# Performance work log

Hardware: AMD Instinct MI355X
Metric: run time of the kernel (lower is better)

## Reference

```python
import jax, jax.numpy as jnp
import numpy as np

N, E, IN_DIM, HID, HEADS, OUT_DIM, T = 50000, 200000, 32, 64, 4, 32, 3
NEG_SLOPE = 0.2  # PyG GATv2Conv default


def setup_inputs() -> dict:
    key = jax.random.key(0)
    ks = jax.random.split(key, 16)
    s = 0.1
    return {
        "feat": jax.random.normal(ks[0], (N, IN_DIM), jnp.float32),
        "W_in": jax.random.normal(ks[1], (IN_DIM, HID), jnp.float32) * s,
        "b_in": jnp.zeros((HID,), jnp.float32),
        "Wl": jax.random.normal(ks[2], (2 * HID, HEADS * HID), jnp.float32) * s,
        "bl": jnp.zeros((HEADS * HID,), jnp.float32),
        "Wr": jax.random.normal(ks[3], (2 * HID, HEADS * HID), jnp.float32) * s,
        "br": jnp.zeros((HEADS * HID,), jnp.float32),
        "att": jax.random.normal(ks[4], (HEADS, HID), jnp.float32) * s,
        "b_conv": jnp.zeros((HEADS * HID,), jnp.float32),
        "Wg": jax.random.normal(ks[5], (HID, OUT_DIM), jnp.float32) * s,
        "bg": jnp.zeros((OUT_DIM,), jnp.float32),
        "edge_index": jax.random.randint(ks[6], (2, E), 0, N, jnp.int32),
        "node_mask": jax.random.randint(ks[7], (N,), 0, T + 1, jnp.int32),
        "current_state": jax.random.randint(ks[8], (N,), 0, 2, jnp.int32),
    }


def reference(feat, W_in, b_in, Wl, bl, Wr, br, att, b_conv, Wg, bg,
              edge_index, node_mask, current_state):
    # add self loops (GATv2Conv add_self_loops=True)
    loops = jnp.arange(N, dtype=edge_index.dtype)
    src = jnp.concatenate([edge_index[0], loops])  # [E+N]
    dst = jnp.concatenate([edge_index[1], loops])

    h0 = feat @ W_in + b_in  # [N, HID]
    bias_sum = b_conv.reshape(HEADS, HID).sum(0)  # heads are summed after bias add

    def step(h, i):
        active = node_mask > i  # [N] bool: nodes updated at this step
        x = jnp.concatenate([h, h0], axis=-1)  # [N, 2*HID]
        xl = (x @ Wl + bl).reshape(N, HEADS, HID)  # source transform
        xr = (x @ Wr + br).reshape(N, HEADS, HID)  # target transform
        e_act = active[src] & active[dst]  # edge alive iff both endpoints active
        s = jax.nn.leaky_relu(xl[src] + xr[dst], NEG_SLOPE)  # [E+N, H, C]
        score = jnp.einsum('ehc,hc->eh', s, att)  # [E+N, H]
        score = jnp.where(e_act[:, None], score, -1e30)
        smax = jax.lax.stop_gradient(
            jax.ops.segment_max(score, dst, num_segments=N))  # [N, H]
        ex = jnp.exp(score - smax[dst]) * e_act[:, None].astype(score.dtype)
        denom = jax.ops.segment_sum(ex, dst, num_segments=N)  # [N, H]
        alpha = ex / jnp.maximum(denom[dst], 1e-16)  # segment softmax per dst
        msg = alpha[:, :, None] * xl[src]  # [E+N, H, C]
        agg = jax.ops.segment_sum(msg, dst, num_segments=N)  # [N, H, C]
        out = jnp.tanh(agg.sum(1) + bias_sum)  # sum over heads, then Tanh
        return jnp.where(active[:, None], out, h), None

    h, _ = jax.lax.scan(step, h0, jnp.arange(T))
    # original returns g_embed(h[current_state]); fixed-shape variant: mask rows
    out = (h @ Wg + bg) * (current_state[:, None] > 0).astype(h.dtype)
    return out
```

## Files before the change

### kernel.cpp

```cpp
#include <hip/hip_runtime.h>
#include <hip/hip_bf16.h>

#define NN      50000
#define EE      200000
#define IN_DIM  32
#define HID     64
#define HEADS   4
#define OUTD    32
#define TSTEPS  3

typedef unsigned short bf16_t;
typedef __attribute__((ext_vector_type(8))) short  short8;
typedef __attribute__((ext_vector_type(4))) float  floatx4;

__device__ __forceinline__ float b2f(bf16_t u) {
    union { unsigned int i; float f; } v; v.i = ((unsigned int)u) << 16; return v.f;
}
__device__ __forceinline__ bf16_t f2b(float f) {
    union { float f; unsigned int i; } v; v.f = f;
    unsigned int r = v.i + 0x7FFF + ((v.i >> 16) & 1);
    return (bf16_t)(r >> 16);
}

__global__ __launch_bounds__(256) void k_setup(
        const void* W_in, const void* b_in, const void* att, const void* bconv,
        const void* Wg, const void* bg,
        const void* Wl_raw, const void* Wr_raw, const void* bl_raw, const void* br_raw,
        float* Winf, float* binf, float* attf, float* bcf, float* Wgf, float* bgf,
        bf16_t* __restrict__ Wt, float* __restrict__ bb,
        int* __restrict__ deg, int* __restrict__ flag, int* __restrict__ mbuf) {
    __shared__ int bad;
    int t = threadIdx.x, bid = blockIdx.x;
    if (t == 0) bad = 0;
    __syncthreads();
    {
        const bf16_t* p = (const bf16_t*)W_in;
        int mybad = 0;
        for (int i = t; i < IN_DIM * HID; i += 256) {
            float v = b2f(p[i]);
            if (v != v || fabsf(v) > 100.f) mybad = 1;
        }
        if (mybad) atomicOr(&bad, 1);
    }
    __syncthreads();
    int f = bad ? 0 : 1;
    if (bid == 0 && t == 0) *flag = f;

    if (bid < 256) {
        int i = bid * 256 + t;
        int n = i >> 7, k = i & 127;
        const void* W = (n < 256) ? Wl_raw : Wr_raw;
        int nn = (n < 256) ? n : n - 256;
        float v = f ? b2f(((const bf16_t*)W)[k * 256 + nn])
                    : ((const float*)W)[k * 256 + nn];
        Wt[i] = f2b(v);
        if (k == 0) {
            const void* b = (n < 256) ? bl_raw : br_raw;
            bb[n] = f ? b2f(((const bf16_t*)b)[nn]) : ((const float*)b)[nn];
        }
    } else if (bid < 275) {
        int i = (bid - 256) * 256 + t;
        const void* src; float* dst; int off;
        if      (i < 2048) { src = W_in;  dst = Winf; off = i; }
        else if (i < 2112) { src = b_in;  dst = binf; off = i - 2048; }
        else if (i < 2368) { src = att;   dst = attf; off = i - 2112; }
        else if (i < 2624) { src = bconv; dst = bcf;  off = i - 2368; }
        else if (i < 4672) { src = Wg;    dst = Wgf;  off = i - 2624; }
        else if (i < 4704) { src = bg;    dst = bgf;  off = i - 4672; }
        else return;
        dst[off] = f ? b2f(((const bf16_t*)src)[off]) : ((const float*)src)[off];
    } else {
        int i = (bid - 275) * 256 + t;
        if (i < NN) deg[i] = 0;
        if (bid == 275 && t < 16) mbuf[t] = 0;
    }
}

__global__ __launch_bounds__(256) void k_hist_all(const int* __restrict__ dst,
                                                  const int* __restrict__ mask,
                                                  int* __restrict__ deg,
                                                  int* __restrict__ mbuf) {
    int t = threadIdx.x, bid = blockIdx.x;
    int i = bid * 256 + t;
    if (i < EE) atomicAdd(&deg[dst[i]], 1);
    if (bid < (NN + 255) / 256) {
        __shared__ int wcnt[4][4];
        int wid = t >> 6, lane = t & 63;
        int ni = bid * 256 + t;
        bool valid = ni < NN;
        int v = 0;
        if (valid) { int m = mask[ni]; v = m < 0 ? 0 : (m > 3 ? 3 : m); }
#pragma unroll
        for (int b = 0; b < 4; b++) {
            unsigned long long mm = __ballot(valid && v == b);
            if (lane == 0) wcnt[wid][b] = __popcll(mm);
        }
        __syncthreads();
        if (t < 4) {
            int s = wcnt[0][t] + wcnt[1][t] + wcnt[2][t] + wcnt[3][t];
            if (s) atomicAdd(&mbuf[t], s);
        }
    }
}

__global__ __launch_bounds__(256) void k_scan_partial(const int* __restrict__ deg,
                                                      int* __restrict__ part, int n) {
    __shared__ int sd[256];
    int t = threadIdx.x;
    int base = blockIdx.x * 1024;
    int s = 0;
#pragma unroll
    for (int j = 0; j < 4; j++) {
        int i = base + t * 4 + j;
        if (i < n) s += deg[i];
    }
    sd[t] = s; __syncthreads();
    for (int off = 128; off > 0; off >>= 1) {
        if (t < off) sd[t] += sd[t + off];
        __syncthreads();
    }
    if (t == 0) part[blockIdx.x] = sd[0];
}

__global__ void k_scan_mid(int* part, int nch, int* mbuf) {
    if (threadIdx.x == 0 && blockIdx.x == 0) {
        int acc = 0;
        for (int i = 0; i < nch; i++) { int v = part[i]; part[i] = acc; acc += v; }
        part[nch] = acc;
        int c1 = mbuf[1], c2 = mbuf[2], c3 = mbuf[3];
        mbuf[7] = 0;
        mbuf[6] = c3;
        mbuf[5] = c3 + c2;
        mbuf[4] = c3 + c2 + c1;
        mbuf[8] = c3 + c2 + c1;
        mbuf[9] = c3 + c2;
        mbuf[10] = c3;
    }
}

__global__ __launch_bounds__(256) void k_scan_final(const int* __restrict__ deg,
                                                    const int* __restrict__ part,
                                                    int* __restrict__ row_ptr,
                                                    int* __restrict__ cursor,
                                                    int n, int nch) {
    __shared__ int sc[256];
    int t = threadIdx.x;
    int base = blockIdx.x * 1024;
    int v[4]; int s = 0;
#pragma unroll
    for (int j = 0; j < 4; j++) {
        int i = base + t * 4 + j;
        v[j] = (i < n) ? deg[i] : 0;
        s += v[j];
    }
    sc[t] = s; __syncthreads();
    for (int off = 1; off < 256; off <<= 1) {
        int add = (t >= off) ? sc[t - off] : 0;
        __syncthreads();
        sc[t] += add;
        __syncthreads();
    }
    int run = sc[t] - s + part[blockIdx.x];
#pragma unroll
    for (int j = 0; j < 4; j++) {
        int i = base + t * 4 + j;
        if (i < n) { row_ptr[i] = run; cursor[i] = run; run += v[j]; }
    }
    if (blockIdx.x == 0 && t == 0) row_ptr[n] = part[nch];
}

__global__ __launch_bounds__(256) void k_scatter_all(const int* __restrict__ src,
                                                     const int* __restrict__ dst,
                                                     int* __restrict__ cursor,
                                                     int* __restrict__ col,
                                                     const int* __restrict__ mask,
                                                     int* __restrict__ mbuf,
                                                     int* __restrict__ order) {
    int t = threadIdx.x, bid = blockIdx.x;
    int i = bid * 256 + t;
    if (i < EE) {
        int d = dst[i];
        int pos = atomicAdd(&cursor[d], 1);
        col[pos] = src[i];
    }
    if (bid < (NN + 255) / 256) {
        __shared__ int wcnt[4][4];
        __shared__ int bbase[4];
        int wid = t >> 6, lane = t & 63;
        int ni = bid * 256 + t;
        bool valid = ni < NN;
        int v = 0;
        if (valid) { int m = mask[ni]; v = m < 0 ? 0 : (m > 3 ? 3 : m); }
        int rank = 0;
#pragma unroll
        for (int b = 0; b < 4; b++) {
            unsigned long long mm = __ballot(valid && v == b);
            if (valid && v == b)
                rank = __popcll(mm & ((lane == 0) ? 0ull : (~0ull >> (64 - lane))));
            if (lane == 0) wcnt[wid][b] = __popcll(mm);
        }
        __syncthreads();
        if (t < 4) {
            int tot = wcnt[0][t] + wcnt[1][t] + wcnt[2][t] + wcnt[3][t];
            bbase[t] = atomicAdd(&mbuf[4 + t], tot);
        }
        __syncthreads();
        if (valid) {
            int wpre = 0;
            for (int ww = 0; ww < wid; ww++) wpre += wcnt[ww][v];
            order[bbase[v] + wpre + rank] = ni;
        }
    }
}

__global__ __launch_bounds__(256) void k_h0(const void* __restrict__ feat_raw,
                                            const float* __restrict__ W_in,
                                            const float* __restrict__ b_in,
                                            bf16_t* __restrict__ h0,
                                            bf16_t* __restrict__ h,
                                            const int* __restrict__ flag) {
    __shared__ float Ws[IN_DIM * HID];
    __shared__ float bs[HID];
    int t = threadIdx.x;
    for (int i = t; i < IN_DIM * HID; i += 256) Ws[i] = W_in[i];
    if (t < HID) bs[t] = b_in[t];
    __syncthreads();
    int node = blockIdx.x * 4 + (t >> 6);
    int c = t & 63;
    if (node >= NN) return;
    int f = *flag;
    float acc = bs[c];
    if (f) {
        const bf16_t* fr = (const bf16_t*)feat_raw + (size_t)node * IN_DIM;
#pragma unroll
        for (int k = 0; k < IN_DIM; k++) acc += b2f(fr[k]) * Ws[k * HID + c];
    } else {
        const float* fr = (const float*)feat_raw + (size_t)node * IN_DIM;
#pragma unroll
        for (int k = 0; k < IN_DIM; k++) acc += fr[k] * Ws[k * HID + c];
    }
    bf16_t o = f2b(acc);
    h0[(size_t)node * HID + c] = o;
    h [(size_t)node * HID + c] = o;
}

__global__ __launch_bounds__(256) void k_gemm_mfma(const bf16_t* __restrict__ h,
                                                   const bf16_t* __restrict__ h0,
                                                   const bf16_t* __restrict__ Wt,
                                                   const float* __restrict__ bb,
                                                   bf16_t* __restrict__ xl,
                                                   bf16_t* __restrict__ xr,
                                                   const int* __restrict__ order,
                                                   const int* __restrict__ mbuf,
                                                   int step) {
    int count = mbuf[8 + step];
    int mbase = blockIdx.x * 64;
    if (mbase >= count) return;

    __shared__ bf16_t smem[64 * 136 + 128 * 136];
    bf16_t* As = smem;
    bf16_t* Bs = smem + 64 * 136;
    bf16_t* Cs = smem;

    int t = threadIdx.x;
    int nbase = blockIdx.y * 128;

    {
        int ln = t >> 2, lq = t & 3;
        int idx = mbase + ln;
        int node = (idx < count) ? order[idx] : -1;
        ulonglong2 z; z.x = 0; z.y = 0;
#pragma unroll
        for (int j = 0; j < 2; j++) {
            int chunk = lq + j * 4;
            ulonglong2 vh = z, vh0 = z;
            if (node >= 0) {
                vh  = *(const ulonglong2*)(h  + (size_t)node * HID + chunk * 8);
                vh0 = *(const ulonglong2*)(h0 + (size_t)node * HID + chunk * 8);
            }
            *(ulonglong2*)(&As[ln * 136 + chunk * 8]) = vh;
            *(ulonglong2*)(&As[ln * 136 + 64 + chunk * 8]) = vh0;
        }
    }
#pragma unroll
    for (int i = 0; i < 8; i++) {
        int c = t + i * 256;
        int n = c >> 4, kc = (c & 15) * 8;
        *(ulonglong2*)(&Bs[n * 136 + kc]) =
            *(const ulonglong2*)(Wt + (size_t)(nbase + n) * 128 + kc);
    }
    __syncthreads();

    int wv = t >> 6;
    int lane = t & 63;
    int mrow = lane & 15;
    int quad = lane >> 4;

    floatx4 acc[8];
#pragma unroll
    for (int nf = 0; nf < 8; nf++) acc[nf] = (floatx4){0.f, 0.f, 0.f, 0.f};

#pragma unroll
    for (int kq = 0; kq < 4; kq++) {
        short8 a = *(const short8*)(&As[(wv * 16 + mrow) * 136 + kq * 32 + quad * 8]);
#pragma unroll
        for (int nf = 0; nf < 8; nf++) {
            short8 b = *(const short8*)(&Bs[(nf * 16 + mrow) * 136 + kq * 32 + quad * 8]);
            acc[nf] = __builtin_amdgcn_mfma_f32_16x16x32_bf16(a, b, acc[nf], 0, 0, 0);
        }
    }
    __syncthreads();

#pragma unroll
    for (int nf = 0; nf < 8; nf++) {
        float bv = bb[nbase + nf * 16 + mrow];
#pragma unroll
        for (int r = 0; r < 4; r++) {
            int m = wv * 16 + quad * 4 + r;
            Cs[m * 136 + nf * 16 + mrow] = f2b(acc[nf][r] + bv);
        }
    }
    __syncthreads();

    bf16_t* outp = (blockIdx.y < 2) ? xl : xr;
    int cc = (blockIdx.y & 1) * 128;
#pragma unroll
    for (int i = 0; i < 4; i++) {
        int c = t + i * 256;
        int m = c >> 4, kc = (c & 15) * 8;
        int idx = mbase + m;
        if (idx < count) {
            int node = order[idx];
            *(ulonglong2*)(outp + (size_t)node * 256 + cc + kc) =
                *(const ulonglong2*)(&Cs[m * 136 + kc]);
        }
    }
}

__global__ __launch_bounds__(256) void k_agg(bf16_t* __restrict__ h,
                                             const bf16_t* __restrict__ xl,
                                             const bf16_t* __restrict__ xr,
                                             const float* __restrict__ att,
                                             const float* __restrict__ b_conv,
                                             const int* __restrict__ row_ptr,
                                             const int* __restrict__ col,
                                             const int* __restrict__ node_mask,
                                             const int* __restrict__ order,
                                             const int* __restrict__ mbuf,
                                             int step) {
    int wid = threadIdx.x >> 6;
    int lane = threadIdx.x & 63;
    int idx = blockIdx.x * 4 + wid;
    if (idx >= mbuf[8 + step]) return;
    int node = order[idx];

    float4 attv = *(const float4*)(att + lane * 4);
    ushort4 xru = *(const ushort4*)(xr + (size_t)node * 256 + lane * 4);
    float xr0 = b2f(xru.x), xr1 = b2f(xru.y), xr2 = b2f(xru.z), xr3 = b2f(xru.w);

    float a0 = 0.f, a1 = 0.f, a2 = 0.f, a3 = 0.f, l = 0.f;

    auto edge_body = [&](int s, bool act) {
        if (!act) return;
        ushort4 xu = *(const ushort4*)(xl + (size_t)s * 256 + lane * 4);
        float x0 = b2f(xu.x), x1 = b2f(xu.y), x2 = b2f(xu.z), x3 = b2f(xu.w);
        float v0 = x0 + xr0; v0 = v0 > 0.f ? v0 : 0.2f * v0;
        float v1 = x1 + xr1; v1 = v1 > 0.f ? v1 : 0.2f * v1;
        float v2 = x2 + xr2; v2 = v2 > 0.f ? v2 : 0.2f * v2;
        float v3 = x3 + xr3; v3 = v3 > 0.f ? v3 : 0.2f * v3;
        float part = attv.x * v0 + attv.y * v1 + attv.z * v2 + attv.w * v3;
        part += __shfl_xor(part, 1, 64);
        part += __shfl_xor(part, 2, 64);
        part += __shfl_xor(part, 4, 64);
        part += __shfl_xor(part, 8, 64);
        float p = __expf(part);
        l += p;
        a0 += p * x0; a1 += p * x1; a2 += p * x2; a3 += p * x3;
    };

    edge_body(node, true);
    int e0 = row_ptr[node], e1 = row_ptr[node + 1];
    int e = e0;
    for (; e + 1 < e1; e += 2) {
        int s0 = col[e], s1 = col[e + 1];
        int m0 = node_mask[s0], m1 = node_mask[s1];
        edge_body(s0, m0 > step);
        edge_body(s1, m1 > step);
    }
    if (e < e1) {
        int s0 = col[e];
        edge_body(s0, node_mask[s0] > step);
    }

    float inv = 1.f / l;
    float4 bcv = *(const float4*)(b_conv + lane * 4);
    float t0 = a0 * inv + bcv.x;
    float t1 = a1 * inv + bcv.y;
    float t2 = a2 * inv + bcv.z;
    float t3 = a3 * inv + bcv.w;
    t0 += __shfl_xor(t0, 16, 64); t0 += __shfl_xor(t0, 32, 64);
    t1 += __shfl_xor(t1, 16, 64); t1 += __shfl_xor(t1, 32, 64);
    t2 += __shfl_xor(t2, 16, 64); t2 += __shfl_xor(t2, 32, 64);
    t3 += __shfl_xor(t3, 16, 64); t3 += __shfl_xor(t3, 32, 64);
    if (lane < 16) {
        ushort4 o;
        o.x = f2b(tanhf(t0)); o.y = f2b(tanhf(t1));
        o.z = f2b(tanhf(t2)); o.w = f2b(tanhf(t3));
        *(ushort4*)(h + (size_t)node * HID + lane * 4) = o;
    }
}

__global__ __launch_bounds__(256) void k_out(const bf16_t* __restrict__ h,
                                             const float* __restrict__ Wg,
                                             const float* __restrict__ bg,
                                             const int* __restrict__ cs,
                                             void* __restrict__ out,
                                             const int* __restrict__ flag) {
    __shared__ float Ws[HID * OUTD];
    __shared__ float bs[OUTD];
    int t = threadIdx.x;
    for (int i = t; i < HID * OUTD; i += 256) Ws[i] = Wg[i];
    if (t < OUTD) bs[t] = bg[t];
    __syncthreads();
    int node = blockIdx.x * 8 + (t >> 5);
    int c = t & 31;
    if (node >= NN) return;
    float res = 0.f;
    if (cs[node] > 0) {
        const bf16_t* hr = h + (size_t)node * HID;
        float acc = bs[c];
#pragma unroll
        for (int k = 0; k < HID; k++) acc += b2f(hr[k]) * Ws[k * OUTD + c];
        res = acc;
    }
    size_t idx = (size_t)node * OUTD + c;
    if (*flag) ((bf16_t*)out)[idx] = f2b(res);
    else       ((float*)out)[idx]  = res;
}

static inline size_t alignup(size_t x) { return (x + 255) & ~(size_t)255; }

extern "C" void kernel_launch(void* const* d_in, const int* in_sizes, int n_in,
                              void* d_out, int out_size, void* d_ws, size_t ws_size,
                              hipStream_t stream) {
    const void* feat_raw  = d_in[0];
    const void* W_in_raw  = d_in[1];
    const void* b_in_raw  = d_in[2];
    const void* Wl_raw    = d_in[3];
    const void* bl_raw    = d_in[4];
    const void* Wr_raw    = d_in[5];
    const void* br_raw    = d_in[6];
    const void* att_raw   = d_in[7];
    const void* bconv_raw = d_in[8];
    const void* Wg_raw    = d_in[9];
    const void* bg_raw    = d_in[10];
    const int* edge       = (const int*)d_in[11];
    const int* nmask      = (const int*)d_in[12];
    const int* cstate     = (const int*)d_in[13];

    const int* e_src = edge;
    const int* e_dst = edge + EE;

    const size_t SZ_HB   = alignup((size_t)NN * HID * sizeof(bf16_t));
    const size_t SZ_X    = alignup((size_t)NN * 256 * sizeof(bf16_t));
    const size_t SZ_I    = alignup((size_t)NN * sizeof(int));
    const size_t SZ_RP   = alignup((size_t)(NN + 1) * sizeof(int));
    const size_t SZ_COL  = alignup((size_t)EE * sizeof(int));
    const int nch = (NN + 1023) / 1024;
    const size_t SZ_PART = alignup((size_t)(nch + 1) * sizeof(int));
    const size_t SZ_WIN  = alignup((size_t)IN_DIM * HID * sizeof(float));
    const size_t SZ_WT   = alignup((size_t)512 * 128 * sizeof(bf16_t));
    const size_t SZ_B    = alignup(512 * sizeof(float));
    const size_t SZ_WG   = alignup((size_t)HID * OUTD * sizeof(float));

    char* w = (char*)d_ws;
    bf16_t* h0   = (bf16_t*)w; w += SZ_HB;
    bf16_t* h    = (bf16_t*)w; w += SZ_HB;
    bf16_t* xl   = (bf16_t*)w; w += SZ_X;
    bf16_t* xr   = (bf16_t*)w; w += SZ_X;
    int* deg     = (int*)w;    w += SZ_I;
    int* row_ptr = (int*)w;    w += SZ_RP;
    int* cursor  = (int*)w;    w += SZ_I;
    int* colA    = (int*)w;    w += SZ_COL;
    int* order   = (int*)w;    w += SZ_I;
    int* part    = (int*)w;    w += SZ_PART;
    float* Winf  = (float*)w;  w += SZ_WIN;
    bf16_t* Wt   = (bf16_t*)w; w += SZ_WT;
    float* bb    = (float*)w;  w += SZ_B;
    float* attf  = (float*)w;  w += SZ_B;
    float* bcf   = (float*)w;  w += SZ_B;
    float* Wgf   = (float*)w;  w += SZ_WG;
    float* binf  = (float*)w;  w += SZ_B;
    float* bgf   = (float*)w;  w += SZ_B;
    int* flag    = (int*)w;    w += 256;
    int* mbuf    = (int*)w;    w += 256;
    if ((size_t)(w - (char*)d_ws) > ws_size) return;

    k_setup<<<275 + (NN + 255) / 256, 256, 0, stream>>>(
        W_in_raw, b_in_raw, att_raw, bconv_raw, Wg_raw, bg_raw,
        Wl_raw, Wr_raw, bl_raw, br_raw,
        Winf, binf, attf, bcf, Wgf, bgf, Wt, bb, deg, flag, mbuf);

    k_hist_all<<<(EE + 255) / 256, 256, 0, stream>>>(e_dst, nmask, deg, mbuf);
    k_scan_partial<<<nch, 256, 0, stream>>>(deg, part, NN);
    k_scan_mid<<<1, 64, 0, stream>>>(part, nch, mbuf);
    k_scan_final<<<nch, 256, 0, stream>>>(deg, part, row_ptr, cursor, NN, nch);
    k_scatter_all<<<(EE + 255) / 256, 256, 0, stream>>>(e_src, e_dst, cursor, colA,
                                                        nmask, mbuf, order);

    k_h0<<<(NN + 3) / 4, 256, 0, stream>>>(feat_raw, Winf, binf, h0, h, flag);

    for (int s = 0; s < TSTEPS; s++) {
        k_gemm_mfma<<<dim3((NN + 63) / 64, 4), 256, 0, stream>>>(h, h0, Wt, bb, xl, xr,
                                                                 order, mbuf, s);
        k_agg<<<(NN + 3) / 4, 256, 0, stream>>>(h, xl, xr, attf, bcf,
                                                row_ptr, colA, nmask, order, mbuf, s);
    }

    k_out<<<(NN + 7) / 8, 256, 0, stream>>>(h, Wgf, bgf, cstate, d_out, flag);
}
```

Baseline: 277.8 us.

## Pack source activity level into CSR column bits and grid-stride aggregation

The scatter stage now stores each edge's clamped source node_mask in the top bits of the CSR column entry, so the aggregation kernel no longer does a dependent gather of node_mask per edge. The aggregation kernel becomes a persistent grid-stride loop over 2048 blocks, hoisting the att and bias loads, and unrolls the edge loop by four. This removes one indirect load per edge and the launch cost of blocks that would exit immediately. The packing assumes node ids fit in 28 bits and mask values are clamped to 0..3; with a fixed grid, per-wave load balance depends on how nodes are striped.

```diff
diff --git a/kernel.cpp b/kernel.cpp
--- a/kernel.cpp
+++ b/kernel.cpp
@@ -179,9 +179,11 @@
     int t = threadIdx.x, bid = blockIdx.x;
     int i = bid * 256 + t;
     if (i < EE) {
+        int sv = src[i];
+        int m = mask[sv]; m = m < 0 ? 0 : (m > 3 ? 3 : m);
         int d = dst[i];
         int pos = atomicAdd(&cursor[d], 1);
-        col[pos] = src[i];
+        col[pos] = sv | (m << 28);
     }
     if (bid < (NN + 255) / 256) {
         __shared__ int wcnt[4][4];
@@ -344,69 +346,70 @@
                                              const float* __restrict__ b_conv,
                                              const int* __restrict__ row_ptr,
                                              const int* __restrict__ col,
-                                             const int* __restrict__ node_mask,
                                              const int* __restrict__ order,
                                              const int* __restrict__ mbuf,
                                              int step) {
+    int count = mbuf[8 + step];
     int wid = threadIdx.x >> 6;
     int lane = threadIdx.x & 63;
-    int idx = blockIdx.x * 4 + wid;
-    if (idx >= mbuf[8 + step]) return;
-    int node = order[idx];
-
     float4 attv = *(const float4*)(att + lane * 4);
-    ushort4 xru = *(const ushort4*)(xr + (size_t)node * 256 + lane * 4);
-    float xr0 = b2f(xru.x), xr1 = b2f(xru.y), xr2 = b2f(xru.z), xr3 = b2f(xru.w);
-
-    float a0 = 0.f, a1 = 0.f, a2 = 0.f, a3 = 0.f, l = 0.f;
-
-    auto edge_body = [&](int s, bool act) {
-        if (!act) return;
-        ushort4 xu = *(const ushort4*)(xl + (size_t)s * 256 + lane * 4);
-        float x0 = b2f(xu.x), x1 = b2f(xu.y), x2 = b2f(xu.z), x3 = b2f(xu.w);
-        float v0 = x0 + xr0; v0 = v0 > 0.f ? v0 : 0.2f * v0;
-        float v1 = x1 + xr1; v1 = v1 > 0.f ? v1 : 0.2f * v1;
-        float v2 = x2 + xr2; v2 = v2 > 0.f ? v2 : 0.2f * v2;
-        float v3 = x3 + xr3; v3 = v3 > 0.f ? v3 : 0.2f * v3;
-        float part = attv.x * v0 + attv.y * v1 + attv.z * v2 + attv.w * v3;
-        part += __shfl_xor(part, 1, 64);
-        part += __shfl_xor(part, 2, 64);
-        part += __shfl_xor(part, 4, 64);
-        part += __shfl_xor(part, 8, 64);
-        float p = __expf(part);
-        l += p;
-        a0 += p * x0; a1 += p * x1; a2 += p * x2; a3 += p * x3;
-    };
-
-    edge_body(node, true);
-    int e0 = row_ptr[node], e1 = row_ptr[node + 1];
-    int e = e0;
-    for (; e + 1 < e1; e += 2) {
-        int s0 = col[e], s1 = col[e + 1];
-        int m0 = node_mask[s0], m1 = node_mask[s1];
-        edge_body(s0, m0 > step);
-        edge_body(s1, m1 > step);
-    }
-    if (e < e1) {
-        int s0 = col[e];
-        edge_body(s0, node_mask[s0] > step);
-    }
-
-    float inv = 1.f / l;
-    float4 bcv = *(const float4*)(b_conv + lane * 4);
-    float t0 = a0 * inv + bcv.x;
-    float t1 = a1 * inv + bcv.y;
-    float t2 = a2 * inv + bcv.z;
-    float t3 = a3 * inv + bcv.w;
-    t0 += __shfl_xor(t0, 16, 64); t0 += __shfl_xor(t0, 32, 64);
-    t1 += __shfl_xor(t1, 16, 64); t1 += __shfl_xor(t1, 32, 64);
-    t2 += __shfl_xor(t2, 16, 64); t2 += __shfl_xor(t2, 32, 64);
-    t3 += __shfl_xor(t3, 16, 64); t3 += __shfl_xor(t3, 32, 64);
-    if (lane < 16) {
-        ushort4 o;
-        o.x = f2b(tanhf(t0)); o.y = f2b(tanhf(t1));
-        o.z = f2b(tanhf(t2)); o.w = f2b(tanhf(t3));
-        *(ushort4*)(h + (size_t)node * HID + lane * 4) = o;
+    float4 bcv  = *(const float4*)(b_conv + lane * 4);
+
+    for (int idx = blockIdx.x * 4 + wid; idx < count; idx += gridDim.x * 4) {
+        int node = order[idx];
+
+        ushort4 xru = *(const ushort4*)(xr + (size_t)node * 256 + lane * 4);
+        float xr0 = b2f(xru.x), xr1 = b2f(xru.y), xr2 = b2f(xru.z), xr3 = b2f(xru.w);
+
+        float a0 = 0.f, a1 = 0.f, a2 = 0.f, a3 = 0.f, l = 0.f;
+
+        auto do_edge = [&](int s) {
+            ushort4 xu = *(const ushort4*)(xl + (size_t)s * 256 + lane * 4);
+            float x0 = b2f(xu.x), x1 = b2f(xu.y), x2 = b2f(xu.z), x3 = b2f(xu.w);
+            float v0 = x0 + xr0; v0 = v0 > 0.f ? v0 : 0.2f * v0;
+            float v1 = x1 + xr1; v1 = v1 > 0.f ? v1 : 0.2f * v1;
+            float v2 = x2 + xr2; v2 = v2 > 0.f ? v2 : 0.2f * v2;
+            float v3 = x3 + xr3; v3 = v3 > 0.f ? v3 : 0.2f * v3;
+            float part = attv.x * v0 + attv.y * v1 + attv.z * v2 + attv.w * v3;
+            part += __shfl_xor(part, 1, 64);
+            part += __shfl_xor(part, 2, 64);
+            part += __shfl_xor(part, 4, 64);
+            part += __shfl_xor(part, 8, 64);
+            float p = __expf(part);
+            l += p;
+            a0 += p * x0; a1 += p * x1; a2 += p * x2; a3 += p * x3;
+        };
+
+        do_edge(node);
+        int e0 = row_ptr[node], e1 = row_ptr[node + 1];
+        int e = e0;
+        for (; e + 3 < e1; e += 4) {
+            int c0 = col[e], c1 = col[e + 1], c2 = col[e + 2], c3 = col[e + 3];
+            if (((unsigned)c0 >> 28) > (unsigned)step) do_edge(c0 & 0x0FFFFFFF);
+            if (((unsigned)c1 >> 28) > (unsigned)step) do_edge(c1 & 0x0FFFFFFF);
+            if (((unsigned)c2 >> 28) > (unsigned)step) do_edge(c2 & 0x0FFFFFFF);
+            if (((unsigned)c3 >> 28) > (unsigned)step) do_edge(c3 & 0x0FFFFFFF);
+        }
+        for (; e < e1; e++) {
+            int c = col[e];
+            if (((unsigned)c >> 28) > (unsigned)step) do_edge(c & 0x0FFFFFFF);
+        }
+
+        float inv = 1.f / l;
+        float t0 = a0 * inv + bcv.x;
+        float t1 = a1 * inv + bcv.y;
+        float t2 = a2 * inv + bcv.z;
+        float t3 = a3 * inv + bcv.w;
+        t0 += __shfl_xor(t0, 16, 64); t0 += __shfl_xor(t0, 32, 64);
+        t1 += __shfl_xor(t1, 16, 64); t1 += __shfl_xor(t1, 32, 64);
+        t2 += __shfl_xor(t2, 16, 64); t2 += __shfl_xor(t2, 32, 64);
+        t3 += __shfl_xor(t3, 16, 64); t3 += __shfl_xor(t3, 32, 64);
+        if (lane < 16) {
+            ushort4 o;
+            o.x = f2b(tanhf(t0)); o.y = f2b(tanhf(t1));
+            o.z = f2b(tanhf(t2)); o.w = f2b(tanhf(t3));
+            *(ushort4*)(h + (size_t)node * HID + lane * 4) = o;
+        }
     }
 }
 
@@ -513,8 +516,8 @@
     for (int s = 0; s < TSTEPS; s++) {
         k_gemm_mfma<<<dim3((NN + 63) / 64, 4), 256, 0, stream>>>(h, h0, Wt, bb, xl, xr,
                                                                  order, mbuf, s);
-        k_agg<<<(NN + 3) / 4, 256, 0, stream>>>(h, xl, xr, attf, bcf,
-                                                row_ptr, colA, nmask, order, mbuf, s);
+        k_agg<<<2048, 256, 0, stream>>>(h, xl, xr, attf, bcf,
+                                        row_ptr, colA, order, mbuf, s);
     }
 
     k_out<<<(NN + 7) / 8, 256, 0, stream>>>(h, Wgf, bgf, cstate, d_out, flag);
```

After: 271.1 us. 2.4% less time.
